# Performance work log

Measured on AMD Instinct MI355X. Metric: run time of the kernel, lower is better.

## Reference

```python
import jax, jax.numpy as jnp
import numpy as np

N = 1_000_000          # points
C_IN = 10              # decorated point features
C_OUT = 64             # pillar feature channels
S = 30_000             # number of pillars (segments)
EPS = 1e-3             # BatchNorm1d eps


def setup_inputs() -> dict:
    key = jax.random.key(0)
    ks = jax.random.split(key, 8)
    inputs = jax.random.normal(ks[0], (N, C_IN), dtype=jnp.float32)
    # every pillar gets ~N/S points; sorted, all segments non-empty
    unq_inv = jnp.sort(jnp.arange(N, dtype=jnp.int32) % S)
    W_lin = jax.random.normal(ks[1], (C_OUT, C_IN), dtype=jnp.float32) * 0.3
    gamma = 1.0 + 0.1 * jax.random.normal(ks[2], (C_OUT,), dtype=jnp.float32)
    beta = 0.1 * jax.random.normal(ks[3], (C_OUT,), dtype=jnp.float32)
    dw1 = jax.random.normal(ks[4], (C_OUT,), dtype=jnp.float32) * 0.5      # depthwise 1x1 conv (groups=C)
    pw1 = jax.random.normal(ks[5], (C_OUT, C_OUT), dtype=jnp.float32) * 0.1  # pointwise 1x1 conv
    dw2 = jax.random.normal(ks[6], (C_OUT,), dtype=jnp.float32) * 0.5
    pw2 = jax.random.normal(ks[7], (C_OUT, C_OUT), dtype=jnp.float32) * 0.1
    return {"inputs": inputs, "unq_inv": unq_inv, "W_lin": W_lin,
            "gamma": gamma, "beta": beta, "dw1": dw1, "pw1": pw1,
            "dw2": dw2, "pw2": pw2}


def reference(inputs, unq_inv, W_lin, gamma, beta, dw1, pw1, dw2, pw2):
    # Linear (no bias) -> BN (training-mode batch stats) -> ReLU
    x = inputs @ W_lin.T                                   # [N, C]
    mu = jnp.mean(x, axis=0)
    var = jnp.mean(jnp.square(x - mu), axis=0)             # biased var, as torch BN
    x = (x - mu) * jax.lax.rsqrt(var + EPS) * gamma + beta
    x = jax.nn.relu(x)

    # MAFF attention: local branch (depthwise scale -> swish -> 1x1 conv)
    s = x * dw1                                            # groups=C 1x1 conv == per-channel scale
    xl = (s * jax.nn.sigmoid(s)) @ pw1.T                   # [N, C]
    # global branch: avg-pool over points -> depthwise scale -> relu -> 1x1 conv
    g = jnp.mean(x, axis=0)                                # [C]
    xg = pw2 @ jax.nn.relu(dw2 * g)                        # [C]
    wei = jax.nn.sigmoid(xl + xg)                          # broadcast [N,C] + [C]
    xi = x * (1.0 + wei)

    # segment reductions keyed by pillar id (scatter_max + scatter_sum)
    x_max = jax.ops.segment_max(xi, unq_inv, num_segments=S,
                                indices_are_sorted=True)
    x_sum = jax.ops.segment_sum(xi, unq_inv, num_segments=S,
                                indices_are_sorted=True)
    return x_max + x_sum                                   # [S, C]
```

## Files before the change

### kernel.cpp

```cpp
#include <hip/hip_runtime.h>
#include <math.h>

#define N_PTS   1000000
#define CI      10
#define C       64
#define NSEG    30000
#define BN_EPS  1e-3f
#define FROFF   31104

#define MSTR 7
#define GOFF 512
#define GSTR 8

using f32x4 = __attribute__((ext_vector_type(4))) float;
using s16x8 = __attribute__((ext_vector_type(8))) short;

__device__ inline short f2bf(float x) {
    unsigned u = __float_as_uint(x);
    unsigned r = (u + 0x7fffu + ((u >> 16) & 1u)) >> 16;
    return (short)r;
}
__device__ inline unsigned pack_trunc(float lo, float hi) {
    return (__float_as_uint(hi) & 0xffff0000u) | (__float_as_uint(lo) >> 16);
}
__device__ inline float frcp(float x) { return __builtin_amdgcn_rcpf(x); }
__device__ inline void lds_fence() {
    asm volatile("s_waitcnt lgkmcnt(0)" ::: "memory");
}

struct Rows { float2 r0, r1, r2, r3; };

__global__ void __launch_bounds__(256) k_moments(const float* __restrict__ inp,
                                                 const int* __restrict__ idx,
                                                 float* __restrict__ ws,
                                                 int* __restrict__ starts) {
    const int tid = threadIdx.x;
    const int stride = gridDim.x * blockDim.x;
    float v[65];
#pragma unroll
    for (int k = 0; k < 65; ++k) v[k] = 0.f;

    int p = blockIdx.x * blockDim.x + tid;
    float2 a0, a1, a2, a3, a4;
    int ic = 0, ip = 0;
    auto ld = [&](int qq) {
        const float2* r2 = (const float2*)(inp + (size_t)qq * CI);
        a0 = r2[0]; a1 = r2[1]; a2 = r2[2]; a3 = r2[3]; a4 = r2[4];
        ic = idx[qq]; ip = (qq > 0) ? idx[qq - 1] : ic;
    };
    if (p < N_PTS) ld(p);
    while (p < N_PTS) {
        float r[CI] = {a0.x, a0.y, a1.x, a1.y, a2.x, a2.y, a3.x, a3.y, a4.x, a4.y};
        const int cc = ic, cp = ip, cq = p;
        const int pn = p + stride;
        if (pn < N_PTS) ld(pn);

#pragma unroll
        for (int i = 0; i < CI; ++i) v[i] += r[i];
        int kk = 10;
#pragma unroll
        for (int i = 0; i < CI; ++i)
#pragma unroll
            for (int j = i; j < CI; ++j) { v[kk] = fmaf(r[i], r[j], v[kk]); ++kk; }

        if (cq == 0) starts[0] = 0;
        else if (cp != cc) starts[cc] = cq;
        p = pn;
    }

#pragma unroll
    for (int k = 0; k < 65; ++k) {
#pragma unroll
        for (int off = 32; off >= 1; off >>= 1)
            v[k] += __shfl_xor(v[k], off, 64);
    }
    __shared__ float red[4 * 65];
    const int wv = tid >> 6, ln = tid & 63;
    if (ln == 0) {
#pragma unroll
        for (int k = 0; k < 65; ++k) red[wv * 65 + k] = v[k];
    }
    __syncthreads();
    if (tid < 65)
        atomicAdd(&ws[MSTR * tid],
                  red[tid] + red[65 + tid] + red[130 + tid] + red[195 + tid]);
}

__global__ void __launch_bounds__(256) k_gstats(const float* __restrict__ inp,
                                                const float* __restrict__ W,
                                                const float* __restrict__ gamma,
                                                const float* __restrict__ beta,
                                                float* __restrict__ ws) {
    const int tid  = threadIdx.x;
    const int wv   = tid >> 6;
    const int lane = tid & 63;
    const int m = lane & 15;
    const int q = lane >> 4;

    __shared__ float wp[C * CI];
    __shared__ float bsh[C];

    if (tid < C) {
        const int c = tid;
        float w[CI];
#pragma unroll
        for (int i = 0; i < CI; ++i) w[i] = W[c * CI + i];
        const float inv_n = 1.f / (float)N_PTS;

        float mu = 0.f;
#pragma unroll
        for (int i = 0; i < CI; ++i) mu = fmaf(w[i], ws[MSTR * i], mu);
        mu *= inv_n;

        float ex2 = 0.f;
        int kk = 10;
#pragma unroll
        for (int i = 0; i < CI; ++i)
#pragma unroll
            for (int j = i; j < CI; ++j) {
                float mm = ws[MSTR * kk];
                float t = w[i] * w[j] * mm;
                ex2 += (i == j) ? t : 2.f * t;
                ++kk;
            }
        ex2 *= inv_n;

        float var = ex2 - mu * mu;
        float rstd = rsqrtf(var + BN_EPS);
        float a = rstd * gamma[c];
        float b = beta[c] - mu * a;
        bsh[c] = b;
#pragma unroll
        for (int i = 0; i < CI; ++i) wp[c * CI + i] = a * w[i];
    }
    __syncthreads();

    s16x8 wfr[4];
#pragma unroll
    for (int nt = 0; nt < 4; ++nt) {
        s16x8 t;
#pragma unroll
        for (int j = 0; j < 8; ++j) {
            int k = 8 * q + j;
            t[j] = (k < CI) ? f2bf(wp[(nt * 16 + m) * CI + k]) : (short)0;
        }
        wfr[nt] = t;
    }
    float bb[4];
#pragma unroll
    for (int nt = 0; nt < 4; ++nt) bb[nt] = bsh[nt * 16 + m];

    const int wid = blockIdx.x * 4 + wv;
    const int nw  = gridDim.x * 4;
    const int NB  = N_PTS / 16;

    auto loadrows = [&](int pb) -> Rows {
        Rows R;
        R.r0 = R.r1 = R.r2 = R.r3 = make_float2(0.f, 0.f);
        const float* row = inp + (size_t)(pb + m) * CI;
        if (q == 0) {
            R.r0 = *(const float2*)(row);     R.r1 = *(const float2*)(row + 2);
            R.r2 = *(const float2*)(row + 4); R.r3 = *(const float2*)(row + 6);
        } else if (q == 1) {
            R.r0 = *(const float2*)(row + 8);
        }
        return R;
    };

    float sm[4] = {0.f, 0.f, 0.f, 0.f};
    const f32x4 zero = {0.f, 0.f, 0.f, 0.f};

    Rows A  = loadrows(wid * 16);
    Rows Bv = loadrows((wid + nw) * 16);
    for (int b = wid; b < NB; b += nw) {
        Rows L = A; A = Bv;
        if (b + 2 * nw < NB) Bv = loadrows((b + 2 * nw) * 16);

        union { s16x8 v; unsigned u[4]; } t;
        t.v = s16x8{0, 0, 0, 0, 0, 0, 0, 0};
        if (q < 2) t.u[0] = pack_trunc(L.r0.x, L.r0.y);
        if (q == 0) {
            t.u[1] = pack_trunc(L.r1.x, L.r1.y);
            t.u[2] = pack_trunc(L.r2.x, L.r2.y);
            t.u[3] = pack_trunc(L.r3.x, L.r3.y);
        }

#pragma unroll
        for (int nt = 0; nt < 4; ++nt) {
            f32x4 xt = __builtin_amdgcn_mfma_f32_16x16x32_bf16(t.v, wfr[nt], zero, 0, 0, 0);
#pragma unroll
            for (int r = 0; r < 4; ++r)
                sm[nt] += fmaxf(xt[r] + bb[nt], 0.f);
        }
    }

#pragma unroll
    for (int nt = 0; nt < 4; ++nt) {
        sm[nt] += __shfl_xor(sm[nt], 16, 64);
        sm[nt] += __shfl_xor(sm[nt], 32, 64);
    }
    float S = sm[0];
    if (q == 1) S = sm[1];
    if (q == 2) S = sm[2];
    if (q == 3) S = sm[3];

    __shared__ float red[4 * 64];
    red[wv * 64 + lane] = S;
    __syncthreads();
    if (tid < 64)
        atomicAdd(&ws[GOFF + GSTR * tid],
                  red[tid] + red[64 + tid] + red[128 + tid] + red[192 + tid]);
}

__global__ void k_prep(const float* __restrict__ W,
                       const float* __restrict__ gamma,
                       const float* __restrict__ beta,
                       const float* __restrict__ dw1,
                       const float* __restrict__ pw1,
                       const float* __restrict__ dw2,
                       const float* __restrict__ pw2,
                       float* __restrict__ ws) {
    const int lane = threadIdx.x;
    const int m = lane & 15, q = lane >> 4;
    const float inv_n = 1.f / (float)N_PTS;

    __shared__ float WP[C * CI];
    __shared__ float BSH[C], T[C], XG[C];

    {
        float w[CI];
#pragma unroll
        for (int i = 0; i < CI; ++i) w[i] = W[lane * CI + i];
        float mu = 0.f;
#pragma unroll
        for (int i = 0; i < CI; ++i) mu = fmaf(w[i], ws[MSTR * i], mu);
        mu *= inv_n;
        float ex2 = 0.f;
        int kk = 10;
#pragma unroll
        for (int i = 0; i < CI; ++i)
#pragma unroll
            for (int j = i; j < CI; ++j) {
                float mm = ws[MSTR * kk];
                float t = w[i] * w[j] * mm;
                ex2 += (i == j) ? t : 2.f * t;
                ++kk;
            }
        ex2 *= inv_n;
        float var = ex2 - mu * mu;
        float rstd = rsqrtf(var + BN_EPS);
        float a = rstd * gamma[lane];
        BSH[lane] = beta[lane] - mu * a;
#pragma unroll
        for (int i = 0; i < CI; ++i) WP[lane * CI + i] = a * w[i];
        T[lane] = fmaxf(dw2[lane] * (ws[GOFF + GSTR * lane] * inv_n), 0.f);
    }
    __syncthreads();

    {
        float acc = 0.f;
#pragma unroll
        for (int k = 0; k < C; ++k) acc = fmaf(pw2[lane * C + k], T[k], acc);
        XG[lane] = acc;
    }
    __syncthreads();

    float4* FR = (float4*)(ws + FROFF);
    union { float4 f; s16x8 v; } u;

#pragma unroll
    for (int nt = 0; nt < 4; ++nt) {
        s16x8 tt;
#pragma unroll
        for (int j = 0; j < 8; ++j) {
            int k = 8 * q + j;
            tt[j] = (k < CI) ? f2bf(WP[(nt * 16 + m) * CI + k]) : (short)0;
        }
        u.v = tt; FR[nt * 64 + lane] = u.f;
    }
#pragma unroll
    for (int nt = 0; nt < 4; ++nt)
#pragma unroll
        for (int kc = 0; kc < 2; ++kc) {
            const float* src = pw1 + (nt * 16 + m) * C + kc * 32 + q * 8;
            float4 p0 = *(const float4*)src, p1 = *(const float4*)(src + 4);
            s16x8 tt;
            tt[0] = f2bf(p0.x); tt[1] = f2bf(p0.y); tt[2] = f2bf(p0.z); tt[3] = f2bf(p0.w);
            tt[4] = f2bf(p1.x); tt[5] = f2bf(p1.y); tt[6] = f2bf(p1.z); tt[7] = f2bf(p1.w);
            u.v = tt; FR[(4 + nt * 2 + kc) * 64 + lane] = u.f;
        }
    float4 f;
    f.x = BSH[m]; f.y = BSH[16 + m]; f.z = BSH[32 + m]; f.w = BSH[48 + m];
    FR[12 * 64 + lane] = f;
    f.x = dw1[m]; f.y = dw1[16 + m]; f.z = dw1[32 + m]; f.w = dw1[48 + m];
    FR[13 * 64 + lane] = f;
    f.x = XG[m]; f.y = XG[16 + m]; f.z = XG[32 + m]; f.w = XG[48 + m];
    FR[14 * 64 + lane] = f;
}

#define LD 68
#define TILE (16 * LD)
#define SEGW 4
__global__ void __launch_bounds__(128) k_main(const float* __restrict__ inp,
                                              const float* __restrict__ ws,
                                              const int* __restrict__ starts,
                                              float* __restrict__ out) {
    const int tid  = threadIdx.x;
    const int wv   = tid >> 6;
    const int lane = tid & 63;
    const int m = lane & 15;
    const int q = lane >> 4;
    const f32x4 zero = {0.f, 0.f, 0.f, 0.f};

    const float4* FR = (const float4*)(ws + FROFF);
    union { float4 f; s16x8 v; } u;
    s16x8 wfr[4];
#pragma unroll
    for (int nt = 0; nt < 4; ++nt) { u.f = FR[nt * 64 + lane]; wfr[nt] = u.v; }
    s16x8 bfr[4][2];
#pragma unroll
    for (int nt = 0; nt < 4; ++nt)
#pragma unroll
        for (int kc = 0; kc < 2; ++kc) { u.f = FR[(4 + nt * 2 + kc) * 64 + lane]; bfr[nt][kc] = u.v; }
    const float4 bb4  = FR[12 * 64 + lane];
    const float4 d14  = FR[13 * 64 + lane];
    const float4 xg4  = FR[14 * 64 + lane];
    const float bb[4]  = {bb4.x, bb4.y, bb4.z, bb4.w};
    const float d1v[4] = {d14.x, d14.y, d14.z, d14.w};
    const float xgv[4] = {xg4.x, xg4.y, xg4.z, xg4.w};

    __shared__ float sb[2][2 * TILE];
    float* const tbase = sb[wv];

    const int w  = blockIdx.x * 2 + wv;
    const int s0 = w * SEGW;

    const int start = starts[s0];
    int end_cur = starts[s0 + 1];
    int n2 = starts[s0 + 2];
    int n3 = starts[s0 + 3];
    int n4 = (s0 + 4 < NSEG) ? starts[s0 + 4] : N_PTS;
    const int end_all = n4;

    int cur = s0;

    float sm[4]  = {0.f, 0.f, 0.f, 0.f};
    float mxv[4] = {-INFINITY, -INFINITY, -INFINITY, -INFINITY};

    auto flushseg = [&](int s) {
#pragma unroll
        for (int nt = 0; nt < 4; ++nt) {
            sm[nt] += __shfl_xor(sm[nt], 16, 64);
            sm[nt] += __shfl_xor(sm[nt], 32, 64);
            mxv[nt] = fmaxf(mxv[nt], __shfl_xor(mxv[nt], 16, 64));
            mxv[nt] = fmaxf(mxv[nt], __shfl_xor(mxv[nt], 32, 64));
        }
        float S = sm[0], M = mxv[0];
        if (q == 1) { S = sm[1]; M = mxv[1]; }
        if (q == 2) { S = sm[2]; M = mxv[2]; }
        if (q == 3) { S = sm[3]; M = mxv[3]; }
        out[(size_t)s * C + lane] = S + M;
#pragma unroll
        for (int nt = 0; nt < 4; ++nt) { sm[nt] = 0.f; mxv[nt] = -INFINITY; }
    };

    auto advance = [&]() {
        end_cur = n2; n2 = n3; n3 = n4;
    };

    auto loadrows = [&](int pb) -> Rows {
        Rows R;
        R.r0 = R.r1 = R.r2 = R.r3 = make_float2(0.f, 0.f);
        const float* row = inp + (size_t)min(pb + m, N_PTS - 1) * CI;
        if (q == 0) {
            R.r0 = *(const float2*)(row);     R.r1 = *(const float2*)(row + 2);
            R.r2 = *(const float2*)(row + 4); R.r3 = *(const float2*)(row + 6);
        } else if (q == 1) {
            R.r0 = *(const float2*)(row + 8);
        }
        return R;
    };

    Rows A = loadrows(start);
    Rows B = (start + 16 < end_all) ? loadrows(start + 16) : A;

    int tog = 0;
    for (int base = start; base < end_all; base += 16, tog ^= 1) {
        float* const my = tbase + tog * TILE;
        Rows L = A;
        A = B;
        if (base + 32 < end_all) B = loadrows(base + 32);

        const int nb = min(16, end_all - base);

        union { s16x8 v; unsigned uu[4]; } t;
        t.v = s16x8{0, 0, 0, 0, 0, 0, 0, 0};
        if (q < 2) t.uu[0] = pack_trunc(L.r0.x, L.r0.y);
        if (q == 0) {
            t.uu[1] = pack_trunc(L.r1.x, L.r1.y);
            t.uu[2] = pack_trunc(L.r2.x, L.r2.y);
            t.uu[3] = pack_trunc(L.r3.x, L.r3.y);
        }

        f32x4 xt[4];
#pragma unroll
        for (int nt = 0; nt < 4; ++nt)
            xt[nt] = __builtin_amdgcn_mfma_f32_16x16x32_bf16(t.v, wfr[nt], zero, 0, 0, 0);

        float xn[4][4];
#pragma unroll
        for (int nt = 0; nt < 4; ++nt)
#pragma unroll
            for (int r = 0; r < 4; ++r) {
                float x = fmaxf(xt[nt][r] + bb[nt], 0.f);
                xn[nt][r] = x;
                float sg = x * d1v[nt];
                float sw = sg * frcp(1.f + __expf(-sg));
                my[(4 * q + r) * LD + nt * 16 + m] = sw;
            }
        lds_fence();

        s16x8 av[2];
#pragma unroll
        for (int kc = 0; kc < 2; ++kc) {
            const float* src = &my[m * LD + kc * 32 + q * 8];
            float4 p0 = *(const float4*)src;
            float4 p1 = *(const float4*)(src + 4);
            union { s16x8 v; unsigned uu[4]; } tt;
            tt.uu[0] = pack_trunc(p0.x, p0.y);
            tt.uu[1] = pack_trunc(p0.z, p0.w);
            tt.uu[2] = pack_trunc(p1.x, p1.y);
            tt.uu[3] = pack_trunc(p1.z, p1.w);
            av[kc] = tt.v;
        }

        f32x4 xi[4];
#pragma unroll
        for (int nt = 0; nt < 4; ++nt) {
            xi[nt] = __builtin_amdgcn_mfma_f32_16x16x32_bf16(av[0], bfr[nt][0], zero, 0, 0, 0);
            xi[nt] = __builtin_amdgcn_mfma_f32_16x16x32_bf16(av[1], bfr[nt][1], xi[nt], 0, 0, 0);
        }

#pragma unroll
        for (int nt = 0; nt < 4; ++nt)
#pragma unroll
            for (int r = 0; r < 4; ++r) {
                float v   = xi[nt][r] + xgv[nt];
                float wei = frcp(1.f + __expf(-v));
                float x   = xn[nt][r];
                xi[nt][r] = fmaf(x, wei, x);
            }

        const int fin = base + nb;
        if (fin <= end_cur) {
            if (nb == 16) {
#pragma unroll
                for (int nt = 0; nt < 4; ++nt)
#pragma unroll
                    for (int r = 0; r < 4; ++r) {
                        sm[nt] += xi[nt][r];
                        mxv[nt] = fmaxf(mxv[nt], xi[nt][r]);
                    }
            } else {
#pragma unroll
                for (int nt = 0; nt < 4; ++nt)
#pragma unroll
                    for (int r = 0; r < 4; ++r) {
                        bool act = (4 * q + r) < nb;
                        sm[nt] += act ? xi[nt][r] : 0.f;
                        mxv[nt] = fmaxf(mxv[nt], act ? xi[nt][r] : -INFINITY);
                    }
            }
            if (fin == end_cur) { flushseg(cur); ++cur; advance(); }
        } else {
            const int Bn = end_cur - base;
#pragma unroll
            for (int nt = 0; nt < 4; ++nt)
#pragma unroll
                for (int r = 0; r < 4; ++r) {
                    bool act = (4 * q + r) < Bn;
                    sm[nt] += act ? xi[nt][r] : 0.f;
                    mxv[nt] = fmaxf(mxv[nt], act ? xi[nt][r] : -INFINITY);
                }
            flushseg(cur); ++cur;
#pragma unroll
            for (int nt = 0; nt < 4; ++nt)
#pragma unroll
                for (int r = 0; r < 4; ++r) {
                    int pt = 4 * q + r;
                    bool act = (pt >= Bn) && (pt < nb);
                    sm[nt] += act ? xi[nt][r] : 0.f;
                    mxv[nt] = fmaxf(mxv[nt], act ? xi[nt][r] : -INFINITY);
                }
            advance();
        }
    }
}

extern "C" void kernel_launch(void* const* d_in, const int* in_sizes, int n_in,
                              void* d_out, int out_size, void* d_ws, size_t ws_size,
                              hipStream_t stream) {
    const float* inp   = (const float*)d_in[0];
    const int*   unq   = (const int*)d_in[1];
    const float* W     = (const float*)d_in[2];
    const float* gamma = (const float*)d_in[3];
    const float* beta  = (const float*)d_in[4];
    const float* dw1   = (const float*)d_in[5];
    const float* pw1   = (const float*)d_in[6];
    const float* dw2   = (const float*)d_in[7];
    const float* pw2   = (const float*)d_in[8];
    float* out = (float*)d_out;
    float* ws  = (float*)d_ws;
    int* starts = (int*)ws + 1024;

    hipMemsetAsync(ws, 0, 1024 * sizeof(float), stream);

    k_moments <<<1024, 256, 0, stream>>>(inp, unq, ws, starts);
    k_gstats  <<<1024, 256, 0, stream>>>(inp, W, gamma, beta, ws);
    k_prep    <<<1,    64,  0, stream>>>(W, gamma, beta, dw1, pw1, dw2, pw2, ws);
    k_main    <<<3750, 128, 0, stream>>>(inp, ws, starts, out);
}
```

Before: 264.0 us.

## Fold prep into gstats last block, store swish tile as bf16, 2 segs/wave

Removes the single-block k_prep launch by having the last finishing block of k_gstats (detected with an atomic counter) compute the global-branch vector and pack the MFMA fragments. The main kernel now writes the swish activations to LDS as truncated bf16 shorts and reads the MFMA A-operand directly, halving LDS traffic and dropping the repacking. It also changes the work split to 2 segments per wave with 4 waves per 256-thread block. The risks are a serialized tail in the last block and shorter per-wave streams with less prefetch overlap.

```diff
diff --git a/kernel.cpp b/kernel.cpp
--- a/kernel.cpp
+++ b/kernel.cpp
@@ -11,6 +11,7 @@
 #define MSTR 7
 #define GOFF 512
 #define GSTR 8
+#define CTRI 961
 
 using f32x4 = __attribute__((ext_vector_type(4))) float;
 using s16x8 = __attribute__((ext_vector_type(8))) short;
@@ -90,6 +91,10 @@
                                                 const float* __restrict__ W,
                                                 const float* __restrict__ gamma,
                                                 const float* __restrict__ beta,
+                                                const float* __restrict__ dw1,
+                                                const float* __restrict__ pw1,
+                                                const float* __restrict__ dw2,
+                                                const float* __restrict__ pw2,
                                                 float* __restrict__ ws) {
     const int tid  = threadIdx.x;
     const int wv   = tid >> 6;
@@ -210,98 +215,70 @@
     if (tid < 64)
         atomicAdd(&ws[GOFF + GSTR * tid],
                   red[tid] + red[64 + tid] + red[128 + tid] + red[192 + tid]);
-}
-
-__global__ void k_prep(const float* __restrict__ W,
-                       const float* __restrict__ gamma,
-                       const float* __restrict__ beta,
-                       const float* __restrict__ dw1,
-                       const float* __restrict__ pw1,
-                       const float* __restrict__ dw2,
-                       const float* __restrict__ pw2,
-                       float* __restrict__ ws) {
-    const int lane = threadIdx.x;
-    const int m = lane & 15, q = lane >> 4;
+
+    __shared__ int lastf;
+    __syncthreads();
+    if (tid == 0) {
+        __threadfence();
+        int old = atomicAdd((int*)ws + CTRI, 1);
+        lastf = (old == (int)gridDim.x - 1);
+    }
+    __syncthreads();
+    if (!lastf) return;
+    __threadfence();
+
+    __shared__ float T[C], XG[C];
     const float inv_n = 1.f / (float)N_PTS;
-
-    __shared__ float WP[C * CI];
-    __shared__ float BSH[C], T[C], XG[C];
-
-    {
-        float w[CI];
-#pragma unroll
-        for (int i = 0; i < CI; ++i) w[i] = W[lane * CI + i];
-        float mu = 0.f;
-#pragma unroll
-        for (int i = 0; i < CI; ++i) mu = fmaf(w[i], ws[MSTR * i], mu);
-        mu *= inv_n;
-        float ex2 = 0.f;
-        int kk = 10;
-#pragma unroll
-        for (int i = 0; i < CI; ++i)
-#pragma unroll
-            for (int j = i; j < CI; ++j) {
-                float mm = ws[MSTR * kk];
-                float t = w[i] * w[j] * mm;
-                ex2 += (i == j) ? t : 2.f * t;
-                ++kk;
-            }
-        ex2 *= inv_n;
-        float var = ex2 - mu * mu;
-        float rstd = rsqrtf(var + BN_EPS);
-        float a = rstd * gamma[lane];
-        BSH[lane] = beta[lane] - mu * a;
-#pragma unroll
-        for (int i = 0; i < CI; ++i) WP[lane * CI + i] = a * w[i];
-        T[lane] = fmaxf(dw2[lane] * (ws[GOFF + GSTR * lane] * inv_n), 0.f);
-    }
-    __syncthreads();
-
-    {
+    if (tid < 64)
+        T[tid] = fmaxf(dw2[tid] * (ws[GOFF + GSTR * tid] * inv_n), 0.f);
+    __syncthreads();
+    if (tid < 64) {
         float acc = 0.f;
 #pragma unroll
-        for (int k = 0; k < C; ++k) acc = fmaf(pw2[lane * C + k], T[k], acc);
-        XG[lane] = acc;
-    }
-    __syncthreads();
-
-    float4* FR = (float4*)(ws + FROFF);
-    union { float4 f; s16x8 v; } u;
-
-#pragma unroll
-    for (int nt = 0; nt < 4; ++nt) {
-        s16x8 tt;
-#pragma unroll
-        for (int j = 0; j < 8; ++j) {
-            int k = 8 * q + j;
-            tt[j] = (k < CI) ? f2bf(WP[(nt * 16 + m) * CI + k]) : (short)0;
-        }
-        u.v = tt; FR[nt * 64 + lane] = u.f;
-    }
-#pragma unroll
-    for (int nt = 0; nt < 4; ++nt)
-#pragma unroll
-        for (int kc = 0; kc < 2; ++kc) {
-            const float* src = pw1 + (nt * 16 + m) * C + kc * 32 + q * 8;
-            float4 p0 = *(const float4*)src, p1 = *(const float4*)(src + 4);
+        for (int k = 0; k < C; ++k) acc = fmaf(pw2[tid * C + k], T[k], acc);
+        XG[tid] = acc;
+    }
+    __syncthreads();
+
+    if (tid < 64) {
+        float4* FR = (float4*)(ws + FROFF);
+        union { float4 f; s16x8 v; } u;
+
+#pragma unroll
+        for (int nt = 0; nt < 4; ++nt) {
             s16x8 tt;
-            tt[0] = f2bf(p0.x); tt[1] = f2bf(p0.y); tt[2] = f2bf(p0.z); tt[3] = f2bf(p0.w);
-            tt[4] = f2bf(p1.x); tt[5] = f2bf(p1.y); tt[6] = f2bf(p1.z); tt[7] = f2bf(p1.w);
-            u.v = tt; FR[(4 + nt * 2 + kc) * 64 + lane] = u.f;
-        }
-    float4 f;
-    f.x = BSH[m]; f.y = BSH[16 + m]; f.z = BSH[32 + m]; f.w = BSH[48 + m];
-    FR[12 * 64 + lane] = f;
-    f.x = dw1[m]; f.y = dw1[16 + m]; f.z = dw1[32 + m]; f.w = dw1[48 + m];
-    FR[13 * 64 + lane] = f;
-    f.x = XG[m]; f.y = XG[16 + m]; f.z = XG[32 + m]; f.w = XG[48 + m];
-    FR[14 * 64 + lane] = f;
-}
-
-#define LD 68
-#define TILE (16 * LD)
-#define SEGW 4
-__global__ void __launch_bounds__(128) k_main(const float* __restrict__ inp,
+#pragma unroll
+            for (int j = 0; j < 8; ++j) {
+                int k = 8 * q + j;
+                tt[j] = (k < CI) ? f2bf(wp[(nt * 16 + m) * CI + k]) : (short)0;
+            }
+            u.v = tt; FR[nt * 64 + lane] = u.f;
+        }
+#pragma unroll
+        for (int nt = 0; nt < 4; ++nt)
+#pragma unroll
+            for (int kc = 0; kc < 2; ++kc) {
+                const float* src = pw1 + (nt * 16 + m) * C + kc * 32 + q * 8;
+                float4 p0 = *(const float4*)src, p1 = *(const float4*)(src + 4);
+                s16x8 tt;
+                tt[0] = f2bf(p0.x); tt[1] = f2bf(p0.y); tt[2] = f2bf(p0.z); tt[3] = f2bf(p0.w);
+                tt[4] = f2bf(p1.x); tt[5] = f2bf(p1.y); tt[6] = f2bf(p1.z); tt[7] = f2bf(p1.w);
+                u.v = tt; FR[(4 + nt * 2 + kc) * 64 + lane] = u.f;
+            }
+        float4 f;
+        f.x = bsh[m]; f.y = bsh[16 + m]; f.z = bsh[32 + m]; f.w = bsh[48 + m];
+        FR[12 * 64 + lane] = f;
+        f.x = dw1[m]; f.y = dw1[16 + m]; f.z = dw1[32 + m]; f.w = dw1[48 + m];
+        FR[13 * 64 + lane] = f;
+        f.x = XG[m]; f.y = XG[16 + m]; f.z = XG[32 + m]; f.w = XG[48 + m];
+        FR[14 * 64 + lane] = f;
+    }
+}
+
+#define LD2 72
+#define TILE2 (16 * LD2)
+#define SEGW 2
+__global__ void __launch_bounds__(256) k_main(const float* __restrict__ inp,
                                               const float* __restrict__ ws,
                                               const int* __restrict__ starts,
                                               float* __restrict__ out) {
@@ -329,20 +306,19 @@
     const float d1v[4] = {d14.x, d14.y, d14.z, d14.w};
     const float xgv[4] = {xg4.x, xg4.y, xg4.z, xg4.w};
 
-    __shared__ float sb[2][2 * TILE];
-    float* const tbase = sb[wv];
-
-    const int w  = blockIdx.x * 2 + wv;
+    __shared__ short sb16[4][2 * TILE2];
+    short* const tbase = sb16[wv];
+
+    const int w  = blockIdx.x * 4 + wv;
     const int s0 = w * SEGW;
 
     const int start = starts[s0];
-    int end_cur = starts[s0 + 1];
-    int n2 = starts[s0 + 2];
-    int n3 = starts[s0 + 3];
-    int n4 = (s0 + 4 < NSEG) ? starts[s0 + 4] : N_PTS;
-    const int end_all = n4;
+    const int st1 = starts[s0 + 1];
+    const int st2 = (s0 + 2 < NSEG) ? starts[s0 + 2] : N_PTS;
+    const int end_all = st2;
 
     int cur = s0;
+    int end_cur = st1;
 
     float sm[4]  = {0.f, 0.f, 0.f, 0.f};
     float mxv[4] = {-INFINITY, -INFINITY, -INFINITY, -INFINITY};
@@ -362,10 +338,6 @@
         out[(size_t)s * C + lane] = S + M;
 #pragma unroll
         for (int nt = 0; nt < 4; ++nt) { sm[nt] = 0.f; mxv[nt] = -INFINITY; }
-    };
-
-    auto advance = [&]() {
-        end_cur = n2; n2 = n3; n3 = n4;
     };
 
     auto loadrows = [&](int pb) -> Rows {
@@ -386,7 +358,7 @@
 
     int tog = 0;
     for (int base = start; base < end_all; base += 16, tog ^= 1) {
-        float* const my = tbase + tog * TILE;
+        short* const myt = tbase + tog * TILE2;
         Rows L = A;
         A = B;
         if (base + 32 < end_all) B = loadrows(base + 32);
@@ -416,23 +388,15 @@
                 xn[nt][r] = x;
                 float sg = x * d1v[nt];
                 float sw = sg * frcp(1.f + __expf(-sg));
-                my[(4 * q + r) * LD + nt * 16 + m] = sw;
+                myt[(4 * q + r) * LD2 + nt * 16 + m] =
+                    (short)(__float_as_uint(sw) >> 16);
             }
         lds_fence();
 
         s16x8 av[2];
 #pragma unroll
-        for (int kc = 0; kc < 2; ++kc) {
-            const float* src = &my[m * LD + kc * 32 + q * 8];
-            float4 p0 = *(const float4*)src;
-            float4 p1 = *(const float4*)(src + 4);
-            union { s16x8 v; unsigned uu[4]; } tt;
-            tt.uu[0] = pack_trunc(p0.x, p0.y);
-            tt.uu[1] = pack_trunc(p0.z, p0.w);
-            tt.uu[2] = pack_trunc(p1.x, p1.y);
-            tt.uu[3] = pack_trunc(p1.z, p1.w);
-            av[kc] = tt.v;
-        }
+        for (int kc = 0; kc < 2; ++kc)
+            av[kc] = *(const s16x8*)(myt + m * LD2 + kc * 32 + q * 8);
 
         f32x4 xi[4];
 #pragma unroll
@@ -471,7 +435,7 @@
                         mxv[nt] = fmaxf(mxv[nt], act ? xi[nt][r] : -INFINITY);
                     }
             }
-            if (fin == end_cur) { flushseg(cur); ++cur; advance(); }
+            if (fin == end_cur) { flushseg(cur); ++cur; end_cur = st2; }
         } else {
             const int Bn = end_cur - base;
 #pragma unroll
@@ -492,7 +456,7 @@
                     sm[nt] += act ? xi[nt][r] : 0.f;
                     mxv[nt] = fmaxf(mxv[nt], act ? xi[nt][r] : -INFINITY);
                 }
-            advance();
+            end_cur = st2;
         }
     }
 }
@@ -516,7 +480,6 @@
     hipMemsetAsync(ws, 0, 1024 * sizeof(float), stream);
 
     k_moments <<<1024, 256, 0, stream>>>(inp, unq, ws, starts);
-    k_gstats  <<<1024, 256, 0, stream>>>(inp, W, gamma, beta, ws);
-    k_prep    <<<1,    64,  0, stream>>>(W, gamma, beta, dw1, pw1, dw2, pw2, ws);
-    k_main    <<<3750, 128, 0, stream>>>(inp, ws, starts, out);
-}
+    k_gstats  <<<1024, 256, 0, stream>>>(inp, W, gamma, beta, dw1, pw1, dw2, pw2, ws);
+    k_main    <<<3750, 256, 0, stream>>>(inp, ws, starts, out);
+}
```

After: 282.7 us. 1.07x slower.
